# Kernel optimization log

Hardware: AMD Instinct MI355X
Metric: run time of the kernel (lower is better)

Reference implementation:

```python
import jax, jax.numpy as jnp
import numpy as np

B, P, K, H, W = 32, 8, 17, 192, 192
ALPHA = 0.5
TEMP = 2.0
SIGMA = 3.0


def _bce_with_logits_mean(x, t):
    # numerically stable BCEWithLogitsLoss, reduction='mean'
    return jnp.mean(jnp.maximum(x, 0.0) - x * t + jnp.log1p(jnp.exp(-jnp.abs(x))))


def _kl_batchmean(s_logprob, t_prob):
    # torch KLDivLoss(reduction='batchmean'): sum(t * (log t - log s)) / batch
    return jnp.sum(t_prob * (jnp.log(t_prob) - s_logprob)) / s_logprob.shape[0]


def _keypoints_loss(pred, kps, vis):
    # pred: [B,K,H,W]; kps: [B,P,K,2] normalized; vis: [B,P,K] int
    b, k, h, w = pred.shape
    x = jnp.floor(kps[..., 0] * (w - 1))  # [B,P,K]; coords>=0 so floor == int()
    y = jnp.floor(kps[..., 1] * (h - 1))
    valid = ((vis > 0) & (x >= 0) & (x < w) & (y >= 0) & (y < h)).astype(pred.dtype)
    inv2s2 = 1.0 / (2.0 * SIGMA * SIGMA)
    ax = jnp.arange(w, dtype=pred.dtype)
    ay = jnp.arange(h, dtype=pred.dtype)
    # separable Gaussian: exp(-((a-x)^2+(b-y)^2)/2s^2) = gx(a)*gy(b)
    gx = jnp.exp(-(ax - x[..., None]) ** 2 * inv2s2) * valid[..., None]  # [B,P,K,W]
    gy = jnp.exp(-(ay - y[..., None]) ** 2 * inv2s2)                     # [B,P,K,H]
    # original indexes target[k][a,b] with a over grid_x (W axis); H==W required
    target = jnp.einsum('bpkw,bpkh->bkwh', gx, gy)  # [B,K,W,H] == [B,K,H,W]
    per = jnp.sum((pred - target) ** 2, axis=(1, 2, 3))          # F.mse_loss sum
    denom = jnp.sum(vis, axis=(1, 2)).astype(pred.dtype) + 1e-6
    return jnp.mean(per / denom)


def setup_inputs() -> dict:
    key = jax.random.key(0)
    k1, k2, k3, k4, k5, k6, k7 = jax.random.split(key, 7)
    return {
        's_seg_logits': jax.random.normal(k1, (B, 1, H, W), dtype=jnp.float32),
        's_pose_logits': jax.random.normal(k2, (B, K, H, W), dtype=jnp.float32),
        't_seg_logits': jax.random.normal(k3, (B, 1, H, W), dtype=jnp.float32),
        't_pose_logits': jax.random.normal(k4, (B, K, H, W), dtype=jnp.float32),
        'mask': jax.random.uniform(k5, (B, H, W), dtype=jnp.float32),
        'keypoints': jax.random.uniform(k6, (B, P, K, 2), dtype=jnp.float32),
        'visibilities': jax.random.randint(k7, (B, P, K), 0, 2, dtype=jnp.int32),
    }


def reference(s_seg_logits, s_pose_logits, t_seg_logits, t_pose_logits, mask, keypoints, visibilities):
    # task losses
    task_seg = _bce_with_logits_mean(s_seg_logits, mask[:, None])  # unsqueeze(1)
    task_pose = _keypoints_loss(s_pose_logits, keypoints, visibilities)
    task_loss = task_seg + task_pose
    # segmentation distillation (softmax over channel dim)
    s_seg_lp = jax.nn.log_softmax(s_seg_logits / TEMP, axis=1)
    t_seg_p = jax.nn.softmax(t_seg_logits / TEMP, axis=1)
    seg_distill = _kl_batchmean(s_seg_lp, t_seg_p) * TEMP ** 2
    # pose distillation (softmax over flattened K*H*W)
    s_pose_lp = jax.nn.log_softmax(s_pose_logits.reshape(s_pose_logits.shape[0], -1) / TEMP, axis=1)
    t_pose_p = jax.nn.softmax(t_pose_logits.reshape(t_pose_logits.shape[0], -1) / TEMP, axis=1)
    pose_distill = _kl_batchmean(s_pose_lp, t_pose_p) * TEMP ** 2
    distill_loss = seg_distill + pose_distill
    total = ALPHA * distill_loss + (1.0 - ALPHA) * task_loss
    return total
```

## Files before the change

### kernel.cpp

```cpp
#include <hip/hip_runtime.h>
#include <math.h>

#define B_   32
#define P_   8
#define K_   17
#define H_   192
#define W_   192
#define HW_  (H_*W_)
#define NBK  (B_*K_)

#define STREAM_PER_B 153
#define STREAM_BLKS  (B_*STREAM_PER_B)
#define STAMP_BLKS   (B_*K_*P_)
#define TSQ_BLKS     NBK
#define BCE_BLKS     96
#define STAMP_BASE   STREAM_BLKS
#define TSQ_BASE     (STAMP_BASE+STAMP_BLKS)
#define BCE_BASE     (TSQ_BASE+TSQ_BLKS)
#define TOTAL_BLKS   (BCE_BASE+BCE_BLKS)

#define RADIUS 18
#define WIN    (2*RADIUS+1)

#define WS_STREAM 0
#define WS_STAMP  20480
#define WS_TSQ    25088
#define WS_BCE    25728

__device__ inline float wave_red_sum(float v) {
    for (int o = 32; o; o >>= 1) v += __shfl_xor(v, o, 64);
    return v;
}

__global__ void __launch_bounds__(256) main_kernel(
        const float* __restrict__ s_pose, const float* __restrict__ t_pose,
        const float* __restrict__ kps,    const int* __restrict__ vis,
        const float* __restrict__ s_seg,  const float* __restrict__ mask,
        float* __restrict__ ws) {
    __shared__ float sred[4][4];
    __shared__ float gx_s[WIN + 3], gy_s[WIN + 3];

    const int blk = blockIdx.x;
    const int tid = threadIdx.x;
    const float inv18 = 1.0f / 18.0f;

    if (blk < STREAM_BLKS) {
        int b = blk / STREAM_PER_B;
        int r = blk - b*STREAM_PER_B;
        const float4* s4 = (const float4*)s_pose + (size_t)b*(STREAM_PER_B*1024) + (size_t)r*1024;
        const float4* t4 = (const float4*)t_pose + (size_t)b*(STREAM_PER_B*1024) + (size_t)r*1024;
        float S2 = 0.f, Zu = 0.f, Zv = 0.f, A = 0.f;
#pragma unroll
        for (int j = 0; j < 4; j++) {
            float4 sv = s4[j*256 + tid];
            float4 tv = t4[j*256 + tid];
            S2 += sv.x*sv.x + sv.y*sv.y + sv.z*sv.z + sv.w*sv.w;
            float u0 = tv.x*0.5f, v0 = sv.x*0.5f;
            float u1 = tv.y*0.5f, v1 = sv.y*0.5f;
            float u2 = tv.z*0.5f, v2 = sv.z*0.5f;
            float u3 = tv.w*0.5f, v3 = sv.w*0.5f;
            float e0 = __expf(u0), e1 = __expf(u1), e2 = __expf(u2), e3 = __expf(u3);
            Zu += (e0 + e1) + (e2 + e3);
            A  += (e0*(u0-v0) + e1*(u1-v1)) + (e2*(u2-v2) + e3*(u3-v3));
            Zv += (__expf(v0) + __expf(v1)) + (__expf(v2) + __expf(v3));
        }
        S2 = wave_red_sum(S2);
        Zu = wave_red_sum(Zu);
        Zv = wave_red_sum(Zv);
        A  = wave_red_sum(A);
        int w = tid >> 6;
        if ((tid & 63) == 0) {
            sred[w][0] = S2; sred[w][1] = Zu; sred[w][2] = Zv; sred[w][3] = A;
        }
        __syncthreads();
        if (tid == 0) {
            float* o = ws + WS_STREAM + (size_t)blk * 4;
            o[0] = sred[0][0] + sred[1][0] + sred[2][0] + sred[3][0];
            o[1] = sred[0][1] + sred[1][1] + sred[2][1] + sred[3][1];
            o[2] = sred[0][2] + sred[1][2] + sred[2][2] + sred[3][2];
            o[3] = sred[0][3] + sred[1][3] + sred[2][3] + sred[3][3];
        }
        return;
    }

    if (blk < TSQ_BASE) {
        int sb  = blk - STAMP_BASE;
        int b   = sb / (K_*P_);
        int rem = sb - b*(K_*P_);
        int k   = rem / P_;
        int p   = rem - k*P_;
        float kx = kps[((b*P_ + p)*K_ + k)*2 + 0];
        float ky = kps[((b*P_ + p)*K_ + k)*2 + 1];
        int   vv = vis[(b*P_ + p)*K_ + k];
        float fx = floorf(kx * (float)(W_-1));
        float fy = floorf(ky * (float)(H_-1));
        bool ok = (vv > 0) && (fx >= 0.f) && (fx < (float)W_) && (fy >= 0.f) && (fy < (float)H_);
        if (!ok) { if (tid == 0) ws[WS_STAMP + sb] = 0.f; return; }
        int X0 = max(0, (int)fx - RADIUS), X1 = min(H_-1, (int)fx + RADIUS);
        int Y0 = max(0, (int)fy - RADIUS), Y1 = min(W_-1, (int)fy + RADIUS);
        int nr = X1 - X0 + 1, nc = Y1 - Y0 + 1;
        if (tid < nr) {
            float d = (float)(X0 + tid) - fx;
            gx_s[tid] = __expf(-d*d*inv18);
        } else if (tid >= 64 && tid - 64 < nc) {
            float d = (float)(Y0 + tid - 64) - fy;
            gy_s[tid - 64] = __expf(-d*d*inv18);
        }
        __syncthreads();
        const float* pb = s_pose + (size_t)(b*K_ + k) * HW_;
        float acc = 0.f;
        int lim = nr << 6;
        for (int e = tid; e < lim; e += 256) {
            int row = e >> 6, col = e & 63;
            if (col < nc)
                acc += pb[(X0 + row)*W_ + (Y0 + col)] * gx_s[row] * gy_s[col];
        }
        acc = wave_red_sum(acc);
        if ((tid & 63) == 0) sred[0][tid >> 6] = acc;
        __syncthreads();
        if (tid == 0)
            ws[WS_STAMP + sb] = sred[0][0] + sred[0][1] + sred[0][2] + sred[0][3];
        return;
    }

    if (blk < BCE_BASE) {
        int sb = blk - TSQ_BASE;
        int b = sb / K_, k = sb - b*K_;
        int pq = tid >> 2, p = pq >> 3, q = pq & 7, ln = tid & 3;
        float kxp = kps[((b*P_ + p)*K_ + k)*2 + 0];
        float kyp = kps[((b*P_ + p)*K_ + k)*2 + 1];
        float kxq = kps[((b*P_ + q)*K_ + k)*2 + 0];
        float kyq = kps[((b*P_ + q)*K_ + k)*2 + 1];
        int vp = vis[(b*P_ + p)*K_ + k];
        int vq = vis[(b*P_ + q)*K_ + k];
        float axp = floorf(kxp * 191.f), ayp = floorf(kyp * 191.f);
        float axq = floorf(kxq * 191.f), ayq = floorf(kyq * 191.f);
        bool okp = (vp > 0) && axp >= 0.f && axp < 192.f && ayp >= 0.f && ayp < 192.f;
        bool okq = (vq > 0) && axq >= 0.f && axq < 192.f && ayq >= 0.f && ayq < 192.f;
        float sx = 0.f, sy = 0.f;
        int i0 = ln * 48;
        for (int i = i0; i < i0 + 48; i++) {
            float da = (float)i - axp, db = (float)i - axq;
            sx += __expf(-(da*da + db*db)*inv18);
            float ea = (float)i - ayp, eb = (float)i - ayq;
            sy += __expf(-(ea*ea + eb*eb)*inv18);
        }
        sx += __shfl_xor(sx, 1, 64); sy += __shfl_xor(sy, 1, 64);
        sx += __shfl_xor(sx, 2, 64); sy += __shfl_xor(sy, 2, 64);
        float val = (ln == 0 && okp && okq) ? sx * sy : 0.f;
        val = wave_red_sum(val);
        if ((tid & 63) == 0) sred[0][tid >> 6] = val;
        __syncthreads();
        if (tid == 0)
            ws[WS_TSQ + sb] = sred[0][0] + sred[0][1] + sred[0][2] + sred[0][3];
        return;
    }

    {
        int bidx = blk - BCE_BASE;
        const float4* x4 = (const float4*)s_seg;
        const float4* m4 = (const float4*)mask;
        size_t base = (size_t)bidx * 3072 + tid;
        float acc = 0.f;
#pragma unroll 4
        for (int j = 0; j < 12; j++) {
            float4 xv = x4[base + j*256];
            float4 tv = m4[base + j*256];
            acc += fmaxf(xv.x, 0.f) - xv.x*tv.x + log1pf(__expf(-fabsf(xv.x)));
            acc += fmaxf(xv.y, 0.f) - xv.y*tv.y + log1pf(__expf(-fabsf(xv.y)));
            acc += fmaxf(xv.z, 0.f) - xv.z*tv.z + log1pf(__expf(-fabsf(xv.z)));
            acc += fmaxf(xv.w, 0.f) - xv.w*tv.w + log1pf(__expf(-fabsf(xv.w)));
        }
        acc = wave_red_sum(acc);
        if ((tid & 63) == 0) sred[0][tid >> 6] = acc;
        __syncthreads();
        if (tid == 0)
            ws[WS_BCE + bidx] = sred[0][0] + sred[0][1] + sred[0][2] + sred[0][3];
    }
}

__global__ void __launch_bounds__(256) finalize_kernel(
        const float* __restrict__ ws, const int* __restrict__ vis,
        float* __restrict__ out) {
    __shared__ float rS2[B_][8], rZu[B_][8], rZv[B_][8], rA[B_][8];
    __shared__ float rCr[B_][8], rTq[B_][8];
    __shared__ int   rVs[B_][8];
    __shared__ float skl[B_], skp[B_];
    __shared__ float bw[4];
    int tid = threadIdx.x;
    int b = tid >> 3, s = tid & 7;

    float S2 = 0.f, Zu = 0.f, Zv = 0.f, A = 0.f, cr = 0.f, tq = 0.f;
    for (int j = s; j < STREAM_PER_B; j += 8) {
        const float* p = ws + WS_STREAM + (size_t)(b*STREAM_PER_B + j) * 4;
        S2 += p[0]; Zu += p[1]; Zv += p[2]; A += p[3];
    }
    for (int j = s; j < K_*P_; j += 8) cr += ws[WS_STAMP + b*(K_*P_) + j];
    for (int j = s; j < K_;    j += 8) tq += ws[WS_TSQ + b*K_ + j];
    int vs = 0;
    for (int m = s; m < P_*K_; m += 8) vs += vis[b*(P_*K_) + m];
    rS2[b][s] = S2; rZu[b][s] = Zu; rZv[b][s] = Zv; rA[b][s] = A;
    rCr[b][s] = cr; rTq[b][s] = tq; rVs[b][s] = vs;

    float bce = (tid < BCE_BLKS) ? ws[WS_BCE + tid] : 0.f;
    bce = wave_red_sum(bce);
    if ((tid & 63) == 0) bw[tid >> 6] = bce;
    __syncthreads();

    if (tid < B_) {
        float tS2=0.f, tZu=0.f, tZv=0.f, tA=0.f, tCr=0.f, tTq=0.f; int tVs=0;
#pragma unroll
        for (int q2 = 0; q2 < 8; q2++) {
            tS2 += rS2[tid][q2]; tZu += rZu[tid][q2]; tZv += rZv[tid][q2];
            tA  += rA[tid][q2];  tCr += rCr[tid][q2]; tTq += rTq[tid][q2];
            tVs += rVs[tid][q2];
        }
        float mse = tS2 - 2.f*tCr + tTq;
        skl[tid] = tA/tZu + (logf(tZv) - logf(tZu));
        skp[tid] = mse / ((float)tVs + 1e-6f);
    }
    __syncthreads();

    if (tid == 0) {
        float kl = 0.f, kpv = 0.f;
        for (int i = 0; i < B_; i++) { kl += skl[i]; kpv += skp[i]; }
        float bsum = bw[0] + bw[1] + bw[2] + bw[3];
        float pose_distill = 4.0f * kl / (float)B_;
        float task_seg  = bsum / (float)(B_ * HW_);
        float task_pose = kpv / (float)B_;
        out[0] = 0.5f * pose_distill + 0.5f * (task_seg + task_pose);
    }
}

extern "C" void kernel_launch(void* const* d_in, const int* in_sizes, int n_in,
                              void* d_out, int out_size, void* d_ws, size_t ws_size,
                              hipStream_t stream) {
    const float* s_seg  = (const float*)d_in[0];
    const float* s_pose = (const float*)d_in[1];
    const float* t_pose = (const float*)d_in[3];
    const float* mask   = (const float*)d_in[4];
    const float* kps    = (const float*)d_in[5];
    const int*   vis    = (const int*)d_in[6];
    float* out = (float*)d_out;
    float* ws  = (float*)d_ws;

    main_kernel<<<TOTAL_BLKS, 256, 0, stream>>>(s_pose, t_pose, kps, vis,
                                                s_seg, mask, ws);
    finalize_kernel<<<1, 256, 0, stream>>>(ws, vis, out);
}
```

Measured before the change: 228.1 us.

## Use persistent fixed grid folding stream, BCE, stamp and TSQ work per block

Replaces the heterogeneous grid of about 9900 specialised blocks with 2048 uniform blocks. Each block streams a strided slice of one batch's pose data, handles a slice of the BCE input, then loops over stamp units and optionally a TSQ unit. The aim is to cut block launch and scheduling overhead and give every block more bytes in flight. The trade-off is that the stamp and TSQ work now runs serially after the streaming work inside the same blocks, which can lengthen the tail.

Result: faster. 216.0 us (-5.3%).

```diff
diff --git a/kernel.cpp b/kernel.cpp
--- a/kernel.cpp
+++ b/kernel.cpp
@@ -7,29 +7,35 @@
 #define H_   192
 #define W_   192
 #define HW_  (H_*W_)
-#define NBK  (B_*K_)
-
-#define STREAM_PER_B 153
-#define STREAM_BLKS  (B_*STREAM_PER_B)
-#define STAMP_BLKS   (B_*K_*P_)
-#define TSQ_BLKS     NBK
-#define BCE_BLKS     96
-#define STAMP_BASE   STREAM_BLKS
-#define TSQ_BASE     (STAMP_BASE+STAMP_BLKS)
-#define BCE_BASE     (TSQ_BASE+TSQ_BLKS)
-#define TOTAL_BLKS   (BCE_BASE+BCE_BLKS)
-
+#define PB4   156672
+#define NBLKS 2048
+#define PER_B_BLKS 64
+#define CHUNK 16384
+#define FULL_IT 9
+#define REM4  9216
+#define BCE4  294912
+
+#define STAMP_UNITS (B_*K_*P_)
+#define TSQ_UNITS   (B_*K_)
 #define RADIUS 18
-#define WIN    (2*RADIUS+1)
-
-#define WS_STREAM 0
-#define WS_STAMP  20480
-#define WS_TSQ    25088
-#define WS_BCE    25728
+
+#define WS_BLK   0
+#define WS_STAMP 16384
+#define WS_TSQ   20736
 
 __device__ inline float wave_red_sum(float v) {
     for (int o = 32; o; o >>= 1) v += __shfl_xor(v, o, 64);
     return v;
+}
+
+__device__ inline void kl_elem(float sv, float tv,
+        float& S2, float& Zu, float& Zv, float& A) {
+    S2 += sv*sv;
+    float u = tv*0.5f, v = sv*0.5f;
+    float eu = __expf(u);
+    Zu += eu;
+    A  += eu*(u - v);
+    Zv += __expf(v);
 }
 
 __global__ void __launch_bounds__(256) main_kernel(
@@ -37,102 +43,120 @@
         const float* __restrict__ kps,    const int* __restrict__ vis,
         const float* __restrict__ s_seg,  const float* __restrict__ mask,
         float* __restrict__ ws) {
-    __shared__ float sred[4][4];
-    __shared__ float gx_s[WIN + 3], gy_s[WIN + 3];
+    __shared__ float sred[4][5];
+    __shared__ float gx_s[40], gy_s[40];
 
     const int blk = blockIdx.x;
     const int tid = threadIdx.x;
     const float inv18 = 1.0f / 18.0f;
 
-    if (blk < STREAM_BLKS) {
-        int b = blk / STREAM_PER_B;
-        int r = blk - b*STREAM_PER_B;
-        const float4* s4 = (const float4*)s_pose + (size_t)b*(STREAM_PER_B*1024) + (size_t)r*1024;
-        const float4* t4 = (const float4*)t_pose + (size_t)b*(STREAM_PER_B*1024) + (size_t)r*1024;
-        float S2 = 0.f, Zu = 0.f, Zv = 0.f, A = 0.f;
-#pragma unroll
-        for (int j = 0; j < 4; j++) {
-            float4 sv = s4[j*256 + tid];
-            float4 tv = t4[j*256 + tid];
-            S2 += sv.x*sv.x + sv.y*sv.y + sv.z*sv.z + sv.w*sv.w;
-            float u0 = tv.x*0.5f, v0 = sv.x*0.5f;
-            float u1 = tv.y*0.5f, v1 = sv.y*0.5f;
-            float u2 = tv.z*0.5f, v2 = sv.z*0.5f;
-            float u3 = tv.w*0.5f, v3 = sv.w*0.5f;
-            float e0 = __expf(u0), e1 = __expf(u1), e2 = __expf(u2), e3 = __expf(u3);
-            Zu += (e0 + e1) + (e2 + e3);
-            A  += (e0*(u0-v0) + e1*(u1-v1)) + (e2*(u2-v2) + e3*(u3-v3));
-            Zv += (__expf(v0) + __expf(v1)) + (__expf(v2) + __expf(v3));
-        }
-        S2 = wave_red_sum(S2);
-        Zu = wave_red_sum(Zu);
-        Zv = wave_red_sum(Zv);
-        A  = wave_red_sum(A);
+    const int b  = blk >> 6;
+    const int lg = ((blk & 63) << 8) | tid;
+    const float4* s4 = (const float4*)s_pose + (size_t)b*PB4 + lg;
+    const float4* t4 = (const float4*)t_pose + (size_t)b*PB4 + lg;
+
+    float S2 = 0.f, Zu = 0.f, Zv = 0.f, A = 0.f;
+#pragma unroll 3
+    for (int j = 0; j < FULL_IT; j++) {
+        float4 sv = s4[(size_t)j*CHUNK];
+        float4 tv = t4[(size_t)j*CHUNK];
+        kl_elem(sv.x, tv.x, S2, Zu, Zv, A);
+        kl_elem(sv.y, tv.y, S2, Zu, Zv, A);
+        kl_elem(sv.z, tv.z, S2, Zu, Zv, A);
+        kl_elem(sv.w, tv.w, S2, Zu, Zv, A);
+    }
+    if (lg < REM4) {
+        float4 sv = s4[(size_t)FULL_IT*CHUNK];
+        float4 tv = t4[(size_t)FULL_IT*CHUNK];
+        kl_elem(sv.x, tv.x, S2, Zu, Zv, A);
+        kl_elem(sv.y, tv.y, S2, Zu, Zv, A);
+        kl_elem(sv.z, tv.z, S2, Zu, Zv, A);
+        kl_elem(sv.w, tv.w, S2, Zu, Zv, A);
+    }
+
+    float bce = 0.f;
+    {
+        int gid = (blk << 8) | tid;
+        if (gid < BCE4) {
+            float4 xv = ((const float4*)s_seg)[gid];
+            float4 mv = ((const float4*)mask)[gid];
+            bce += fmaxf(xv.x, 0.f) - xv.x*mv.x + log1pf(__expf(-fabsf(xv.x)));
+            bce += fmaxf(xv.y, 0.f) - xv.y*mv.y + log1pf(__expf(-fabsf(xv.y)));
+            bce += fmaxf(xv.z, 0.f) - xv.z*mv.z + log1pf(__expf(-fabsf(xv.z)));
+            bce += fmaxf(xv.w, 0.f) - xv.w*mv.w + log1pf(__expf(-fabsf(xv.w)));
+        }
+    }
+
+    S2  = wave_red_sum(S2);
+    Zu  = wave_red_sum(Zu);
+    Zv  = wave_red_sum(Zv);
+    A   = wave_red_sum(A);
+    bce = wave_red_sum(bce);
+    {
         int w = tid >> 6;
         if ((tid & 63) == 0) {
-            sred[w][0] = S2; sred[w][1] = Zu; sred[w][2] = Zv; sred[w][3] = A;
-        }
-        __syncthreads();
-        if (tid == 0) {
-            float* o = ws + WS_STREAM + (size_t)blk * 4;
-            o[0] = sred[0][0] + sred[1][0] + sred[2][0] + sred[3][0];
-            o[1] = sred[0][1] + sred[1][1] + sred[2][1] + sred[3][1];
-            o[2] = sred[0][2] + sred[1][2] + sred[2][2] + sred[3][2];
-            o[3] = sred[0][3] + sred[1][3] + sred[2][3] + sred[3][3];
-        }
-        return;
-    }
-
-    if (blk < TSQ_BASE) {
-        int sb  = blk - STAMP_BASE;
-        int b   = sb / (K_*P_);
-        int rem = sb - b*(K_*P_);
-        int k   = rem / P_;
-        int p   = rem - k*P_;
-        float kx = kps[((b*P_ + p)*K_ + k)*2 + 0];
-        float ky = kps[((b*P_ + p)*K_ + k)*2 + 1];
-        int   vv = vis[(b*P_ + p)*K_ + k];
-        float fx = floorf(kx * (float)(W_-1));
-        float fy = floorf(ky * (float)(H_-1));
-        bool ok = (vv > 0) && (fx >= 0.f) && (fx < (float)W_) && (fy >= 0.f) && (fy < (float)H_);
-        if (!ok) { if (tid == 0) ws[WS_STAMP + sb] = 0.f; return; }
-        int X0 = max(0, (int)fx - RADIUS), X1 = min(H_-1, (int)fx + RADIUS);
-        int Y0 = max(0, (int)fy - RADIUS), Y1 = min(W_-1, (int)fy + RADIUS);
-        int nr = X1 - X0 + 1, nc = Y1 - Y0 + 1;
-        if (tid < nr) {
-            float d = (float)(X0 + tid) - fx;
-            gx_s[tid] = __expf(-d*d*inv18);
-        } else if (tid >= 64 && tid - 64 < nc) {
-            float d = (float)(Y0 + tid - 64) - fy;
-            gy_s[tid - 64] = __expf(-d*d*inv18);
-        }
-        __syncthreads();
-        const float* pb = s_pose + (size_t)(b*K_ + k) * HW_;
+            sred[w][0] = S2; sred[w][1] = Zu; sred[w][2] = Zv;
+            sred[w][3] = A;  sred[w][4] = bce;
+        }
+    }
+    __syncthreads();
+    if (tid == 0) {
+        float* o = ws + WS_BLK + (size_t)blk * 8;
+#pragma unroll
+        for (int c = 0; c < 5; c++)
+            o[c] = sred[0][c] + sred[1][c] + sred[2][c] + sred[3][c];
+    }
+
+    for (int u = blk; u < STAMP_UNITS; u += NBLKS) {
+        __syncthreads();
+        int bb  = u / (K_*P_);
+        int rem = u - bb*(K_*P_);
+        int kk  = rem / P_;
+        int pp  = rem - kk*P_;
+        float kx = kps[((bb*P_ + pp)*K_ + kk)*2 + 0];
+        float ky = kps[((bb*P_ + pp)*K_ + kk)*2 + 1];
+        int   vv = vis[(bb*P_ + pp)*K_ + kk];
+        float fx = floorf(kx * 191.f);
+        float fy = floorf(ky * 191.f);
+        bool ok = (vv > 0) && fx >= 0.f && fx < 192.f && fy >= 0.f && fy < 192.f;
         float acc = 0.f;
-        int lim = nr << 6;
-        for (int e = tid; e < lim; e += 256) {
-            int row = e >> 6, col = e & 63;
-            if (col < nc)
-                acc += pb[(X0 + row)*W_ + (Y0 + col)] * gx_s[row] * gy_s[col];
+        if (ok) {
+            int X0 = max(0, (int)fx - RADIUS), X1 = min(H_-1, (int)fx + RADIUS);
+            int Y0 = max(0, (int)fy - RADIUS), Y1 = min(W_-1, (int)fy + RADIUS);
+            int nr = X1 - X0 + 1, nc = Y1 - Y0 + 1;
+            if (tid < nr) {
+                float d = (float)(X0 + tid) - fx;
+                gx_s[tid] = __expf(-d*d*inv18);
+            } else if (tid >= 64 && tid - 64 < nc) {
+                float d = (float)(Y0 + tid - 64) - fy;
+                gy_s[tid - 64] = __expf(-d*d*inv18);
+            }
+            __syncthreads();
+            const float* pb = s_pose + (size_t)(bb*K_ + kk) * HW_;
+            int lim = nr << 6;
+            for (int e = tid; e < lim; e += 256) {
+                int row = e >> 6, col = e & 63;
+                if (col < nc)
+                    acc += pb[(X0 + row)*W_ + (Y0 + col)] * gx_s[row] * gy_s[col];
+            }
         }
         acc = wave_red_sum(acc);
-        if ((tid & 63) == 0) sred[0][tid >> 6] = acc;
+        if ((tid & 63) == 0) sred[tid >> 6][0] = acc;
         __syncthreads();
         if (tid == 0)
-            ws[WS_STAMP + sb] = sred[0][0] + sred[0][1] + sred[0][2] + sred[0][3];
-        return;
-    }
-
-    if (blk < BCE_BASE) {
-        int sb = blk - TSQ_BASE;
-        int b = sb / K_, k = sb - b*K_;
+            ws[WS_STAMP + u] = sred[0][0] + sred[1][0] + sred[2][0] + sred[3][0];
+    }
+
+    if (blk < TSQ_UNITS) {
+        __syncthreads();
+        int bb = blk / K_, kk = blk - bb*K_;
         int pq = tid >> 2, p = pq >> 3, q = pq & 7, ln = tid & 3;
-        float kxp = kps[((b*P_ + p)*K_ + k)*2 + 0];
-        float kyp = kps[((b*P_ + p)*K_ + k)*2 + 1];
-        float kxq = kps[((b*P_ + q)*K_ + k)*2 + 0];
-        float kyq = kps[((b*P_ + q)*K_ + k)*2 + 1];
-        int vp = vis[(b*P_ + p)*K_ + k];
-        int vq = vis[(b*P_ + q)*K_ + k];
+        float kxp = kps[((bb*P_ + p)*K_ + kk)*2 + 0];
+        float kyp = kps[((bb*P_ + p)*K_ + kk)*2 + 1];
+        float kxq = kps[((bb*P_ + q)*K_ + kk)*2 + 0];
+        float kyq = kps[((bb*P_ + q)*K_ + kk)*2 + 1];
+        int vp = vis[(bb*P_ + p)*K_ + kk];
+        int vq = vis[(bb*P_ + q)*K_ + kk];
         float axp = floorf(kxp * 191.f), ayp = floorf(kyp * 191.f);
         float axq = floorf(kxq * 191.f), ayq = floorf(kyq * 191.f);
         bool okp = (vp > 0) && axp >= 0.f && axp < 192.f && ayp >= 0.f && ayp < 192.f;
@@ -149,33 +173,10 @@
         sx += __shfl_xor(sx, 2, 64); sy += __shfl_xor(sy, 2, 64);
         float val = (ln == 0 && okp && okq) ? sx * sy : 0.f;
         val = wave_red_sum(val);
-        if ((tid & 63) == 0) sred[0][tid >> 6] = val;
+        if ((tid & 63) == 0) sred[tid >> 6][0] = val;
         __syncthreads();
         if (tid == 0)
-            ws[WS_TSQ + sb] = sred[0][0] + sred[0][1] + sred[0][2] + sred[0][3];
-        return;
-    }
-
-    {
-        int bidx = blk - BCE_BASE;
-        const float4* x4 = (const float4*)s_seg;
-        const float4* m4 = (const float4*)mask;
-        size_t base = (size_t)bidx * 3072 + tid;
-        float acc = 0.f;
-#pragma unroll 4
-        for (int j = 0; j < 12; j++) {
-            float4 xv = x4[base + j*256];
-            float4 tv = m4[base + j*256];
-            acc += fmaxf(xv.x, 0.f) - xv.x*tv.x + log1pf(__expf(-fabsf(xv.x)));
-            acc += fmaxf(xv.y, 0.f) - xv.y*tv.y + log1pf(__expf(-fabsf(xv.y)));
-            acc += fmaxf(xv.z, 0.f) - xv.z*tv.z + log1pf(__expf(-fabsf(xv.z)));
-            acc += fmaxf(xv.w, 0.f) - xv.w*tv.w + log1pf(__expf(-fabsf(xv.w)));
-        }
-        acc = wave_red_sum(acc);
-        if ((tid & 63) == 0) sred[0][tid >> 6] = acc;
-        __syncthreads();
-        if (tid == 0)
-            ws[WS_BCE + bidx] = sred[0][0] + sred[0][1] + sred[0][2] + sred[0][3];
+            ws[WS_TSQ + blk] = sred[0][0] + sred[1][0] + sred[2][0] + sred[3][0];
     }
 }
 
@@ -191,8 +192,8 @@
     int b = tid >> 3, s = tid & 7;
 
     float S2 = 0.f, Zu = 0.f, Zv = 0.f, A = 0.f, cr = 0.f, tq = 0.f;
-    for (int j = s; j < STREAM_PER_B; j += 8) {
-        const float* p = ws + WS_STREAM + (size_t)(b*STREAM_PER_B + j) * 4;
+    for (int j = s; j < PER_B_BLKS; j += 8) {
+        const float* p = ws + WS_BLK + (size_t)(b*PER_B_BLKS + j) * 8;
         S2 += p[0]; Zu += p[1]; Zv += p[2]; A += p[3];
     }
     for (int j = s; j < K_*P_; j += 8) cr += ws[WS_STAMP + b*(K_*P_) + j];
@@ -202,7 +203,9 @@
     rS2[b][s] = S2; rZu[b][s] = Zu; rZv[b][s] = Zv; rA[b][s] = A;
     rCr[b][s] = cr; rTq[b][s] = tq; rVs[b][s] = vs;
 
-    float bce = (tid < BCE_BLKS) ? ws[WS_BCE + tid] : 0.f;
+    float bce = 0.f;
+    for (int i = tid; i < NBLKS; i += 256)
+        bce += ws[WS_BLK + (size_t)i * 8 + 4];
     bce = wave_red_sum(bce);
     if ((tid & 63) == 0) bw[tid >> 6] = bce;
     __syncthreads();
@@ -244,7 +247,7 @@
     float* out = (float*)d_out;
     float* ws  = (float*)d_ws;
 
-    main_kernel<<<TOTAL_BLKS, 256, 0, stream>>>(s_pose, t_pose, kps, vis,
-                                                s_seg, mask, ws);
+    main_kernel<<<NBLKS, 256, 0, stream>>>(s_pose, t_pose, kps, vis,
+                                           s_seg, mask, ws);
     finalize_kernel<<<1, 256, 0, stream>>>(ws, vis, out);
 }
```
